# Optimization experiments

Hardware: AMD Instinct MI355X
Metric: run time of the kernel (lower is better)

The kernel has to match this reference:

```python
import jax, jax.numpy as jnp
import numpy as np

N, E, D, L = 100000, 600000, 128, 5
EPS = 1e-5


def setup_inputs() -> dict:
    key = jax.random.key(0)
    ks = jax.random.split(key, 32)
    ri = lambda k, shape, hi: jax.random.randint(k, shape, 0, hi)
    rn = lambda k, shape: jax.random.normal(k, shape, jnp.float32) * 0.02
    inp = {
        'atomic_num': ri(ks[0], (N,), 119),
        'formal_charge': ri(ks[1], (N,), 11),
        'chiral_tag': ri(ks[2], (N,), 5),
        'hybridization': ri(ks[3], (N,), 8),
        'num_explicit_hs': ri(ks[4], (N,), 6),
        'is_aromatic': ri(ks[5], (N,), 2),
        'edge_index': ri(ks[6], (2, E), N),
        'is_conjugated': ri(ks[7], (E,), 2),
        'edge_is_aromatic': ri(ks[8], (E,), 2),
        'bond_type': ri(ks[9], (E,), 22),
        'bond_dir': ri(ks[10], (E,), 7),
        'bond_stereo': ri(ks[11], (E,), 6),
        # atom embedding tables (vocab sizes are typical RDKit cardinalities)
        'emb_atomic_num': rn(ks[12], (120, D)),
        'emb_formal_charge': rn(ks[13], (12, D)),
        'emb_chiral_tag': rn(ks[14], (5, D)),
        'emb_hybridization': rn(ks[15], (8, D)),
        'emb_num_explicit_hs': rn(ks[16], (6, D)),
        'emb_is_aromatic': rn(ks[17], (2, D)),
        # per-layer edge embedding tables, stacked on leading layer axis
        'e_conj': rn(ks[18], (L, 3, D)),
        'e_arom': rn(ks[19], (L, 3, D)),
        'e_btype': rn(ks[20], (L, 23, D)),
        'e_bdir': rn(ks[21], (L, 8, D)),
        'e_bstereo': rn(ks[22], (L, 7, D)),
        # per-layer GIN MLP (D -> 2D -> D)
        'mlp_w1': rn(ks[23], (L, D, 2 * D)),
        'mlp_b1': jnp.zeros((L, 2 * D), jnp.float32),
        'mlp_w2': rn(ks[24], (L, 2 * D, D)),
        'mlp_b2': jnp.zeros((L, D), jnp.float32),
        # per-layer batchnorm affine params (training-mode batch stats)
        'bn_gamma': jnp.ones((L, D), jnp.float32),
        'bn_beta': jnp.zeros((L, D), jnp.float32),
    }
    return inp


def reference(atomic_num, formal_charge, chiral_tag, hybridization,
              num_explicit_hs, is_aromatic, edge_index,
              is_conjugated, edge_is_aromatic, bond_type, bond_dir, bond_stereo,
              emb_atomic_num, emb_formal_charge, emb_chiral_tag,
              emb_hybridization, emb_num_explicit_hs, emb_is_aromatic,
              e_conj, e_arom, e_btype, e_bdir, e_bstereo,
              mlp_w1, mlp_b1, mlp_w2, mlp_b2, bn_gamma, bn_beta):
    # seed node features: sum of atom-feature embeddings  [N, D]
    h = (emb_atomic_num[atomic_num] + emb_formal_charge[formal_charge]
         + emb_chiral_tag[chiral_tag] + emb_hybridization[hybridization]
         + emb_num_explicit_hs[num_explicit_hs] + emb_is_aromatic[is_aromatic])
    src, dst = edge_index[0], edge_index[1]
    for l in range(L):
        # edge embeddings: sum of bond-feature embeddings  [E, D]
        eemb = (e_conj[l][is_conjugated] + e_arom[l][edge_is_aromatic]
                + e_btype[l][bond_type] + e_bdir[l][bond_dir]
                + e_bstereo[l][bond_stereo])
        # self-loop edges use bond-feature index 0 for every feature  [D]
        self_vec = e_conj[l, 0] + e_arom[l, 0] + e_btype[l, 0] + e_bdir[l, 0] + e_bstereo[l, 0]
        # GIN message: x_j + edge_attr, scatter-add at dst; self loops folded in analytically
        msg = h[src] + eemb                                      # [E, D]
        agg = jax.ops.segment_sum(msg, dst, num_segments=N) + h + self_vec
        # GIN update MLP: D -> 2D -> D
        hid = jax.nn.relu(agg @ mlp_w1[l] + mlp_b1[l])
        h = hid @ mlp_w2[l] + mlp_b2[l]
        # batch norm over the node dimension (training-mode batch statistics)
        mean = h.mean(axis=0)
        var = h.var(axis=0)
        h = bn_gamma[l] * (h - mean) * jax.lax.rsqrt(var + EPS) + bn_beta[l]
        if l < L - 1:
            h = jax.nn.relu(h)
        # dropout_ratio = 0.0 -> identity
    return h  # JK='last', graph_pooling=None -> node representations [N, D]
```

## Files before the change

### kernel.cpp

```cpp
#include <hip/hip_runtime.h>

#define NN 100000
#define EE 600000
#define DD 128
#define LL 5
#define CTROWS 5152
#define MBLK 1563
#define GBLK 782
#define SBLK 98

typedef float f32x4 __attribute__((ext_vector_type(4)));
typedef _Float16 f16x8 __attribute__((ext_vector_type(8)));
typedef _Float16 f16x4 __attribute__((ext_vector_type(4)));

__global__ __launch_bounds__(256) void seed_kernel(
    const int* __restrict__ an, const int* __restrict__ fc,
    const int* __restrict__ ct, const int* __restrict__ hy,
    const int* __restrict__ nh, const int* __restrict__ ar,
    const float* __restrict__ ean, const float* __restrict__ efc,
    const float* __restrict__ ect, const float* __restrict__ ehy,
    const float* __restrict__ enh, const float* __restrict__ ear,
    _Float16* __restrict__ h)
{
    int idx = blockIdx.x * 256 + threadIdx.x;
    int n = idx >> 4, q = idx & 15;
    f32x4 a0 = ((const f32x4*)(ean + an[n] * DD))[2 * q];
    f32x4 a1 = ((const f32x4*)(ean + an[n] * DD))[2 * q + 1];
    a0 += ((const f32x4*)(efc + fc[n] * DD))[2 * q];
    a1 += ((const f32x4*)(efc + fc[n] * DD))[2 * q + 1];
    a0 += ((const f32x4*)(ect + ct[n] * DD))[2 * q];
    a1 += ((const f32x4*)(ect + ct[n] * DD))[2 * q + 1];
    a0 += ((const f32x4*)(ehy + hy[n] * DD))[2 * q];
    a1 += ((const f32x4*)(ehy + hy[n] * DD))[2 * q + 1];
    a0 += ((const f32x4*)(enh + nh[n] * DD))[2 * q];
    a1 += ((const f32x4*)(enh + nh[n] * DD))[2 * q + 1];
    a0 += ((const f32x4*)(ear + ar[n] * DD))[2 * q];
    a1 += ((const f32x4*)(ear + ar[n] * DD))[2 * q + 1];
    f16x8 o;
    #pragma unroll
    for (int j = 0; j < 4; ++j) { o[j] = (_Float16)a0[j]; o[j + 4] = (_Float16)a1[j]; }
    ((f16x8*)h)[idx] = o;
}

__global__ __launch_bounds__(256) void convw1_kernel(const float* __restrict__ w1,
                                                     _Float16* __restrict__ w1t)
{
    int idx = blockIdx.x * 256 + threadIdx.x;
    int l = idx >> 15, rem = idx & 32767;
    int n = rem >> 7, k = rem & 127;
    w1t[idx] = (_Float16)w1[l * 32768 + k * 256 + n];
}
__global__ __launch_bounds__(256) void convw2_kernel(const float* __restrict__ w2,
                                                     _Float16* __restrict__ w2t)
{
    int idx = blockIdx.x * 256 + threadIdx.x;
    int l = idx >> 15, rem = idx & 32767;
    int n = rem >> 8, k = rem & 255;
    w2t[idx] = (_Float16)w2[l * 32768 + k * 128 + n];
}

__global__ void idss_kernel(float* __restrict__ idss)
{
    int t = threadIdx.x;
    idss[t] = (t < 128) ? 1.0f : 0.0f;
}

__global__ __launch_bounds__(256) void count_kernel(const int* __restrict__ ei,
                                                    int* __restrict__ cursor)
{
    int e = blockIdx.x * 256 + threadIdx.x;
    if (e < EE) atomicAdd(&cursor[ei[EE + e]], 1);
}

__global__ __launch_bounds__(1024) void btot_kernel(const int* __restrict__ cursor,
                                                    int* __restrict__ btot)
{
    __shared__ int wsum[16];
    int tid = threadIdx.x;
    int i = blockIdx.x * 1024 + tid;
    int x = (i < NN) ? cursor[i] : 0;
    #pragma unroll
    for (int off = 1; off < 64; off <<= 1) x += __shfl_xor(x, off, 64);
    if ((tid & 63) == 0) wsum[tid >> 6] = x;
    __syncthreads();
    if (tid == 0) {
        int s = 0;
        #pragma unroll
        for (int w = 0; w < 16; ++w) s += wsum[w];
        btot[blockIdx.x] = s;
    }
}

__global__ __launch_bounds__(128) void bscan_kernel(const int* __restrict__ btot,
                                                    int* __restrict__ boff,
                                                    int* __restrict__ rowstart)
{
    __shared__ int w0;
    int t = threadIdx.x;
    int lane = t & 63, wv = t >> 6;
    int x = (t < SBLK) ? btot[t] : 0;
    int incl = x;
    #pragma unroll
    for (int off = 1; off < 64; off <<= 1) {
        int u = __shfl_up(incl, off, 64);
        if (lane >= off) incl += u;
    }
    if (wv == 0 && lane == 63) w0 = incl;
    __syncthreads();
    if (wv == 1) incl += w0;
    if (t < SBLK) boff[t] = incl - x;
    if (t == 127) rowstart[NN] = incl;
}

__global__ __launch_bounds__(1024) void apply_kernel(const int* __restrict__ cursorin,
                                                     const int* __restrict__ boff,
                                                     int* __restrict__ rowstart,
                                                     int* __restrict__ cursor)
{
    __shared__ int wsum[16];
    int tid = threadIdx.x;
    int lane = tid & 63, wv = tid >> 6;
    int i = blockIdx.x * 1024 + tid;
    int x = (i < NN) ? cursorin[i] : 0;
    int incl = x;
    #pragma unroll
    for (int off = 1; off < 64; off <<= 1) {
        int u = __shfl_up(incl, off, 64);
        if (lane >= off) incl += u;
    }
    if (lane == 63) wsum[wv] = incl;
    __syncthreads();
    int pre = 0;
    #pragma unroll
    for (int w = 0; w < 16; ++w) pre += (w < wv) ? wsum[w] : 0;
    int excl = boff[blockIdx.x] + pre + incl - x;
    if (i < NN) { rowstart[i] = excl; cursor[i] = excl; }
}

__global__ __launch_bounds__(256) void fill_kernel(
    const int* __restrict__ ei, int* __restrict__ cursor, int* __restrict__ rec,
    const int* __restrict__ f0, const int* __restrict__ f1,
    const int* __restrict__ f2, const int* __restrict__ f3,
    const int* __restrict__ f4)
{
    int e = blockIdx.x * 256 + threadIdx.x;
    if (e >= EE) return;
    int dst = ei[EE + e];
    int p = atomicAdd(&cursor[dst], 1);
    int f = f0[e] + 2 * (f1[e] + 2 * (f2[e] + 23 * (f3[e] + 8 * f4[e])));
    rec[p] = ei[e] | (f << 17);
}

__global__ __launch_bounds__(256) void ctab_kernel(
    const float* __restrict__ ec, const float* __restrict__ ea,
    const float* __restrict__ eb, const float* __restrict__ ed,
    const float* __restrict__ es, _Float16* __restrict__ ctab)
{
    int idx = blockIdx.x * 256 + threadIdx.x;
    int row = idx >> 4, q = idx & 15;
    int conj = row & 1, arom = (row >> 1) & 1;
    int r2 = row >> 2;
    int bt = r2 % 23, r3 = r2 / 23;
    int bd = r3 & 7, bs = r3 >> 3;
    f32x4 a0 = ((const f32x4*)(ec + conj * DD))[2 * q]
             + ((const f32x4*)(ea + arom * DD))[2 * q]
             + ((const f32x4*)(eb + bt * DD))[2 * q]
             + ((const f32x4*)(ed + bd * DD))[2 * q]
             + ((const f32x4*)(es + bs * DD))[2 * q];
    f32x4 a1 = ((const f32x4*)(ec + conj * DD))[2 * q + 1]
             + ((const f32x4*)(ea + arom * DD))[2 * q + 1]
             + ((const f32x4*)(eb + bt * DD))[2 * q + 1]
             + ((const f32x4*)(ed + bd * DD))[2 * q + 1]
             + ((const f32x4*)(es + bs * DD))[2 * q + 1];
    f16x8 o;
    #pragma unroll
    for (int j = 0; j < 4; ++j) { o[j] = (_Float16)a0[j]; o[j + 4] = (_Float16)a1[j]; }
    ((f16x8*)ctab)[idx] = o;
}

__global__ __launch_bounds__(256) void gather_bn_kernel(
    const _Float16* __restrict__ hsrc, _Float16* __restrict__ agg,
    const int* __restrict__ rowstart, const int* __restrict__ rec,
    const _Float16* __restrict__ ctab, const float* __restrict__ ss, int dorelu)
{
    int idx = blockIdx.x * 256 + threadIdx.x;
    int n = idx >> 4, q = idx & 15;
    f32x4 sc0 = ((const f32x4*)ss)[2 * q],        sc1 = ((const f32x4*)ss)[2 * q + 1];
    f32x4 sh0 = ((const f32x4*)(ss + 128))[2 * q], sh1 = ((const f32x4*)(ss + 128))[2 * q + 1];
    int p0 = rowstart[n], p1 = rowstart[n + 1];
    f16x8 x = ((const f16x8*)hsrc)[idx];
    f16x8 c0 = ((const f16x8*)ctab)[q];
    float v[8];
    #pragma unroll
    for (int j = 0; j < 8; ++j) {
        float sc = (j < 4) ? sc0[j] : sc1[j - 4];
        float sh = (j < 4) ? sh0[j] : sh1[j - 4];
        float t = (float)x[j] * sc + sh;
        if (dorelu && t < 0.f) t = 0.f;
        v[j] = t + (float)c0[j];
    }
    if (p0 < p1) {
        int r0 = rec[p0];
        int r1 = (p0 + 1 < p1) ? rec[p0 + 1] : r0;
        f16x8 y0 = *(const f16x8*)(hsrc + (size_t)(r0 & 0x1FFFF) * DD + q * 8);
        f16x8 e0 = *(const f16x8*)(ctab + (size_t)(((unsigned)r0) >> 17) * DD + q * 8);
        for (int p = p0; p < p1; ++p) {
            int r2 = (p + 2 < p1) ? rec[p + 2] : r1;
            f16x8 y1 = *(const f16x8*)(hsrc + (size_t)(r1 & 0x1FFFF) * DD + q * 8);
            f16x8 e1 = *(const f16x8*)(ctab + (size_t)(((unsigned)r1) >> 17) * DD + q * 8);
            #pragma unroll
            for (int j = 0; j < 8; ++j) {
                float sc = (j < 4) ? sc0[j] : sc1[j - 4];
                float sh = (j < 4) ? sh0[j] : sh1[j - 4];
                float t = (float)y0[j] * sc + sh;
                if (dorelu && t < 0.f) t = 0.f;
                v[j] += t + (float)e0[j];
            }
            y0 = y1; e0 = e1; r1 = r2;
        }
    }
    f16x8 o;
    #pragma unroll
    for (int j = 0; j < 8; ++j) o[j] = (_Float16)v[j];
    ((f16x8*)agg)[idx] = o;
}

__global__ __launch_bounds__(256, 2) void mlp_kernel(
    const _Float16* __restrict__ A, const _Float16* __restrict__ w1t,
    const _Float16* __restrict__ w2t,
    const float* __restrict__ b1, const float* __restrict__ b2,
    _Float16* __restrict__ hpre, float* __restrict__ psum, float* __restrict__ psq,
    int M)
{
    __shared__ _Float16 hid[2][8 * 4 * 64 * 8];
    int tid = threadIdx.x;
    int w = tid >> 6, lane = tid & 63;
    int ln = lane & 15, quad = lane >> 4;
    int nodebase = blockIdx.x * 128;
    const f32x4 zero = {0.f, 0.f, 0.f, 0.f};

    f16x8 w1f[4][4];
    #pragma unroll
    for (int n1 = 0; n1 < 4; ++n1)
        #pragma unroll
        for (int kt = 0; kt < 4; ++kt)
            w1f[n1][kt] = *(const f16x8*)(w1t + (w * 64 + n1 * 16 + ln) * 128 + kt * 32 + quad * 8);
    f32x4 b1v[4];
    #pragma unroll
    for (int n1 = 0; n1 < 4; ++n1)
        b1v[n1] = *(const f32x4*)(b1 + w * 64 + n1 * 16 + quad * 4);

    auto gemm1 = [&](int g) {
        int node0 = nodebase + g * 64;
        #pragma unroll
        for (int ns = 0; ns < 4; ++ns) {
            int row = node0 + ns * 16 + ln;
            row = row < M ? row : M - 1;
            f16x8 bact[4];
            #pragma unroll
            for (int kt = 0; kt < 4; ++kt)
                bact[kt] = *(const f16x8*)(A + (size_t)row * 128 + kt * 32 + quad * 8);
            f32x4 acc1[4] = {zero, zero, zero, zero};
            #pragma unroll
            for (int kt = 0; kt < 4; ++kt)
                #pragma unroll
                for (int n1 = 0; n1 < 4; ++n1)
                    acc1[n1] = __builtin_amdgcn_mfma_f32_16x16x32_f16(w1f[n1][kt], bact[kt], acc1[n1], 0, 0, 0);
            #pragma unroll
            for (int n1 = 0; n1 < 4; ++n1) {
                int a = w * 4 + n1;
                f16x4 pk;
                #pragma unroll
                for (int r = 0; r < 4; ++r) {
                    float v = acc1[n1][r] + b1v[n1][r];
                    v = v > 0.f ? v : 0.f;
                    pk[r] = (_Float16)v;
                }
                int lp = ((a & 1) * 2 + (quad >> 1)) * 16 + ln;
                int off = (((a >> 1) * 4 + ns) * 64 + lp) * 8 + (quad & 1) * 4;
                *(f16x4*)(&hid[g][off]) = pk;
            }
        }
    };

    gemm1(0);

    f16x8 w2f[2][8];
    #pragma unroll
    for (int n2 = 0; n2 < 2; ++n2)
        #pragma unroll
        for (int kt2 = 0; kt2 < 8; ++kt2)
            w2f[n2][kt2] = *(const f16x8*)(w2t + (w * 32 + n2 * 16 + ln) * 256 + kt2 * 32 + quad * 8);
    f32x4 b2v[2];
    #pragma unroll
    for (int n2 = 0; n2 < 2; ++n2)
        b2v[n2] = *(const f32x4*)(b2 + w * 32 + n2 * 16 + quad * 4);

    gemm1(1);

    __syncthreads();

    f32x4 ssum[2] = {zero, zero};
    f32x4 sqsum[2] = {zero, zero};
    #pragma unroll
    for (int g = 0; g < 2; ++g) {
        int node0 = nodebase + g * 64;
        #pragma unroll
        for (int ns = 0; ns < 4; ++ns) {
            f32x4 acc2[2] = {zero, zero};
            #pragma unroll
            for (int kt2 = 0; kt2 < 8; ++kt2) {
                f16x8 bf = *(const f16x8*)(&hid[g][((kt2 * 4 + ns) * 64 + lane) * 8]);
                acc2[0] = __builtin_amdgcn_mfma_f32_16x16x32_f16(w2f[0][kt2], bf, acc2[0], 0, 0, 0);
                acc2[1] = __builtin_amdgcn_mfma_f32_16x16x32_f16(w2f[1][kt2], bf, acc2[1], 0, 0, 0);
            }
            int node = node0 + ns * 16 + ln;
            bool valid = node < M;
            #pragma unroll
            for (int n2 = 0; n2 < 2; ++n2) {
                f32x4 v;
                f16x4 pk;
                #pragma unroll
                for (int r = 0; r < 4; ++r) {
                    v[r] = acc2[n2][r] + b2v[n2][r];
                    pk[r] = (_Float16)v[r];
                }
                if (valid) {
                    *(f16x4*)(hpre + (size_t)node * 128 + w * 32 + n2 * 16 + quad * 4) = pk;
                    ssum[n2] += v;
                    sqsum[n2] += v * v;
                }
            }
        }
    }

    #pragma unroll
    for (int n2 = 0; n2 < 2; ++n2)
        #pragma unroll
        for (int off = 1; off < 16; off <<= 1)
            #pragma unroll
            for (int r = 0; r < 4; ++r) {
                ssum[n2][r] += __shfl_xor(ssum[n2][r], off, 64);
                sqsum[n2][r] += __shfl_xor(sqsum[n2][r], off, 64);
            }
    if (ln == 0) {
        #pragma unroll
        for (int n2 = 0; n2 < 2; ++n2) {
            *(f32x4*)(psum + blockIdx.x * 128 + w * 32 + n2 * 16 + quad * 4) = ssum[n2];
            *(f32x4*)(psq + blockIdx.x * 128 + w * 32 + n2 * 16 + quad * 4) = sqsum[n2];
        }
    }
}

__global__ __launch_bounds__(256) void reduce_kernel(
    const float* __restrict__ psum, const float* __restrict__ psq,
    const float* __restrict__ gamma, const float* __restrict__ beta,
    float* __restrict__ ss, int nblk)
{
    int c = blockIdx.x;
    int tid = threadIdx.x;
    float s = 0.f, q = 0.f;
    for (int b = tid; b < nblk; b += 256) {
        s += psum[b * 128 + c];
        q += psq[b * 128 + c];
    }
    #pragma unroll
    for (int off = 1; off < 64; off <<= 1) {
        s += __shfl_xor(s, off, 64);
        q += __shfl_xor(q, off, 64);
    }
    __shared__ float rs[4], rq[4];
    int wave = tid >> 6;
    if ((tid & 63) == 0) { rs[wave] = s; rq[wave] = q; }
    __syncthreads();
    if (tid == 0) {
        s = rs[0] + rs[1] + rs[2] + rs[3];
        q = rq[0] + rq[1] + rq[2] + rq[3];
        const float invN = 1.0f / NN;
        float mean = s * invN;
        float var = q * invN - mean * mean;
        float inv = rsqrtf(var + 1e-5f);
        float scale = gamma[c] * inv;
        ss[c] = scale;
        ss[128 + c] = beta[c] - mean * scale;
    }
}

__global__ __launch_bounds__(256) void final_bn_kernel(
    const _Float16* __restrict__ hpre, float* __restrict__ out,
    const float* __restrict__ ss)
{
    int idx = blockIdx.x * 256 + threadIdx.x;
    int q = idx & 15;
    f16x8 x = ((const f16x8*)hpre)[idx];
    f32x4 sc0 = ((const f32x4*)ss)[2 * q],        sc1 = ((const f32x4*)ss)[2 * q + 1];
    f32x4 sh0 = ((const f32x4*)(ss + 128))[2 * q], sh1 = ((const f32x4*)(ss + 128))[2 * q + 1];
    f32x4 y0, y1;
    #pragma unroll
    for (int j = 0; j < 4; ++j) {
        y0[j] = (float)x[j] * sc0[j] + sh0[j];
        y1[j] = (float)x[j + 4] * sc1[j] + sh1[j];
    }
    ((f32x4*)out)[2 * idx] = y0;
    ((f32x4*)out)[2 * idx + 1] = y1;
}

extern "C" void kernel_launch(void* const* d_in, const int* in_sizes, int n_in,
                              void* d_out, int out_size, void* d_ws, size_t ws_size,
                              hipStream_t stream)
{
    const int* an  = (const int*)d_in[0];
    const int* fc  = (const int*)d_in[1];
    const int* ct  = (const int*)d_in[2];
    const int* hy  = (const int*)d_in[3];
    const int* nh  = (const int*)d_in[4];
    const int* ar  = (const int*)d_in[5];
    const int* ei  = (const int*)d_in[6];
    const int* econ = (const int*)d_in[7];
    const int* earo = (const int*)d_in[8];
    const int* ebt  = (const int*)d_in[9];
    const int* ebd  = (const int*)d_in[10];
    const int* ebs  = (const int*)d_in[11];
    const float* ean = (const float*)d_in[12];
    const float* efc = (const float*)d_in[13];
    const float* ect = (const float*)d_in[14];
    const float* ehy = (const float*)d_in[15];
    const float* enh = (const float*)d_in[16];
    const float* ear = (const float*)d_in[17];
    const float* e_conj   = (const float*)d_in[18];
    const float* e_arom   = (const float*)d_in[19];
    const float* e_btype  = (const float*)d_in[20];
    const float* e_bdir   = (const float*)d_in[21];
    const float* e_bstereo= (const float*)d_in[22];
    const float* mlp_w1 = (const float*)d_in[23];
    const float* mlp_b1 = (const float*)d_in[24];
    const float* mlp_w2 = (const float*)d_in[25];
    const float* mlp_b2 = (const float*)d_in[26];
    const float* bn_gamma = (const float*)d_in[27];
    const float* bn_beta  = (const float*)d_in[28];

    _Float16* h0   = (_Float16*)d_ws;
    _Float16* agg  = h0 + (size_t)NN * DD;
    _Float16* hpre = agg + (size_t)NN * DD;
    _Float16* w1t  = hpre + (size_t)NN * DD;
    _Float16* w2t  = w1t + LL * 256 * 128;
    _Float16* ctab = w2t + LL * 128 * 256;
    float*    psum = (float*)(ctab + CTROWS * DD);
    float*    psq  = psum + MBLK * 128;
    float*    ss   = psq + MBLK * 128;
    float*    idss = ss + 256;
    int* rowstart = (int*)(idss + 256);
    int* cursor   = rowstart + NN + 8;
    int* rec      = cursor + NN;
    int* btot     = rec + EE;
    int* boff     = btot + SBLK + 8;

    convw1_kernel<<<640, 256, 0, stream>>>(mlp_w1, w1t);
    convw2_kernel<<<640, 256, 0, stream>>>(mlp_w2, w2t);
    seed_kernel<<<6250, 256, 0, stream>>>(an, fc, ct, hy, nh, ar,
                                          ean, efc, ect, ehy, enh, ear, h0);
    idss_kernel<<<1, 256, 0, stream>>>(idss);

    hipMemsetAsync(cursor, 0, NN * sizeof(int), stream);
    count_kernel<<<2344, 256, 0, stream>>>(ei, cursor);
    btot_kernel<<<SBLK, 1024, 0, stream>>>(cursor, btot);
    bscan_kernel<<<1, 128, 0, stream>>>(btot, boff, rowstart);
    apply_kernel<<<SBLK, 1024, 0, stream>>>(cursor, boff, rowstart, cursor);
    fill_kernel<<<2344, 256, 0, stream>>>(ei, cursor, rec,
                                          econ, earo, ebt, ebd, ebs);

    for (int l = 0; l < LL; ++l) {
        ctab_kernel<<<322, 256, 0, stream>>>(
            e_conj + l * 3 * DD, e_arom + l * 3 * DD, e_btype + l * 23 * DD,
            e_bdir + l * 8 * DD, e_bstereo + l * 7 * DD, ctab);
        gather_bn_kernel<<<6250, 256, 0, stream>>>(
            (l == 0) ? h0 : hpre, agg, rowstart, rec, ctab,
            (l == 0) ? idss : ss, (l == 0) ? 0 : 1);
        mlp_kernel<<<GBLK, 256, 0, stream>>>(
            agg, w1t + l * 32768, w2t + l * 32768,
            mlp_b1 + l * 256, mlp_b2 + l * 128,
            hpre, psum, psq, NN);
        reduce_kernel<<<128, 256, 0, stream>>>(
            psum, psq, bn_gamma + l * 128, bn_beta + l * 128, ss, GBLK);
    }
    final_bn_kernel<<<6250, 256, 0, stream>>>(hpre, (float*)d_out, ss);
}
```

Baseline: 634.4 us.

## Split MLP kernel across eight waves and single-buffer the hidden tile

The fused GIN MLP kernel now runs 512 threads (8 waves) per block instead of 4. Each wave owns half as many output columns in both GEMMs, which halves the per-wave weight fragments held in registers. The hidden-activation LDS buffer drops from double to single, and the two 64-node groups are processed one after another with barriers between them. This is meant to raise occupancy and latency hiding, at the cost of extra barriers, less overlap between the two GEMMs, and each wave reloading the activation rows.

New measurement: 690.3 us. 8.8% more time.

```diff
diff --git a/kernel.cpp b/kernel.cpp
--- a/kernel.cpp
+++ b/kernel.cpp
@@ -225,33 +225,44 @@
     ((f16x8*)agg)[idx] = o;
 }
 
-__global__ __launch_bounds__(256, 2) void mlp_kernel(
+__global__ __launch_bounds__(512, 2) void mlp_kernel(
     const _Float16* __restrict__ A, const _Float16* __restrict__ w1t,
     const _Float16* __restrict__ w2t,
     const float* __restrict__ b1, const float* __restrict__ b2,
     _Float16* __restrict__ hpre, float* __restrict__ psum, float* __restrict__ psq,
     int M)
 {
-    __shared__ _Float16 hid[2][8 * 4 * 64 * 8];
+    __shared__ _Float16 hid[8 * 4 * 64 * 8];
     int tid = threadIdx.x;
     int w = tid >> 6, lane = tid & 63;
     int ln = lane & 15, quad = lane >> 4;
     int nodebase = blockIdx.x * 128;
     const f32x4 zero = {0.f, 0.f, 0.f, 0.f};
 
-    f16x8 w1f[4][4];
-    #pragma unroll
-    for (int n1 = 0; n1 < 4; ++n1)
+    f16x8 w1f[2][4];
+    #pragma unroll
+    for (int n1 = 0; n1 < 2; ++n1)
         #pragma unroll
         for (int kt = 0; kt < 4; ++kt)
-            w1f[n1][kt] = *(const f16x8*)(w1t + (w * 64 + n1 * 16 + ln) * 128 + kt * 32 + quad * 8);
-    f32x4 b1v[4];
-    #pragma unroll
-    for (int n1 = 0; n1 < 4; ++n1)
-        b1v[n1] = *(const f32x4*)(b1 + w * 64 + n1 * 16 + quad * 4);
-
-    auto gemm1 = [&](int g) {
+            w1f[n1][kt] = *(const f16x8*)(w1t + (w * 32 + n1 * 16 + ln) * 128 + kt * 32 + quad * 8);
+    f32x4 b1v[2];
+    #pragma unroll
+    for (int n1 = 0; n1 < 2; ++n1)
+        b1v[n1] = *(const f32x4*)(b1 + w * 32 + n1 * 16 + quad * 4);
+
+    f16x8 w2f[8];
+    #pragma unroll
+    for (int kt2 = 0; kt2 < 8; ++kt2)
+        w2f[kt2] = *(const f16x8*)(w2t + (w * 16 + ln) * 256 + kt2 * 32 + quad * 8);
+    f32x4 b2v = *(const f32x4*)(b2 + w * 16 + quad * 4);
+
+    f32x4 ssum = zero, sqsum = zero;
+
+    #pragma unroll
+    for (int g = 0; g < 2; ++g) {
         int node0 = nodebase + g * 64;
+        if (g) __syncthreads();
+
         #pragma unroll
         for (int ns = 0; ns < 4; ++ns) {
             int row = node0 + ns * 16 + ln;
@@ -260,15 +271,15 @@
             #pragma unroll
             for (int kt = 0; kt < 4; ++kt)
                 bact[kt] = *(const f16x8*)(A + (size_t)row * 128 + kt * 32 + quad * 8);
-            f32x4 acc1[4] = {zero, zero, zero, zero};
+            f32x4 acc1[2] = {zero, zero};
             #pragma unroll
             for (int kt = 0; kt < 4; ++kt)
                 #pragma unroll
-                for (int n1 = 0; n1 < 4; ++n1)
+                for (int n1 = 0; n1 < 2; ++n1)
                     acc1[n1] = __builtin_amdgcn_mfma_f32_16x16x32_f16(w1f[n1][kt], bact[kt], acc1[n1], 0, 0, 0);
             #pragma unroll
-            for (int n1 = 0; n1 < 4; ++n1) {
-                int a = w * 4 + n1;
+            for (int n1 = 0; n1 < 2; ++n1) {
+                int a = w * 2 + n1;
                 f16x4 pk;
                 #pragma unroll
                 for (int r = 0; r < 4; ++r) {
@@ -278,77 +289,47 @@
                 }
                 int lp = ((a & 1) * 2 + (quad >> 1)) * 16 + ln;
                 int off = (((a >> 1) * 4 + ns) * 64 + lp) * 8 + (quad & 1) * 4;
-                *(f16x4*)(&hid[g][off]) = pk;
+                *(f16x4*)(&hid[off]) = pk;
             }
         }
-    };
-
-    gemm1(0);
-
-    f16x8 w2f[2][8];
-    #pragma unroll
-    for (int n2 = 0; n2 < 2; ++n2)
-        #pragma unroll
-        for (int kt2 = 0; kt2 < 8; ++kt2)
-            w2f[n2][kt2] = *(const f16x8*)(w2t + (w * 32 + n2 * 16 + ln) * 256 + kt2 * 32 + quad * 8);
-    f32x4 b2v[2];
-    #pragma unroll
-    for (int n2 = 0; n2 < 2; ++n2)
-        b2v[n2] = *(const f32x4*)(b2 + w * 32 + n2 * 16 + quad * 4);
-
-    gemm1(1);
-
-    __syncthreads();
-
-    f32x4 ssum[2] = {zero, zero};
-    f32x4 sqsum[2] = {zero, zero};
-    #pragma unroll
-    for (int g = 0; g < 2; ++g) {
-        int node0 = nodebase + g * 64;
+
+        __syncthreads();
+
         #pragma unroll
         for (int ns = 0; ns < 4; ++ns) {
-            f32x4 acc2[2] = {zero, zero};
+            f32x4 acc2 = zero;
             #pragma unroll
             for (int kt2 = 0; kt2 < 8; ++kt2) {
-                f16x8 bf = *(const f16x8*)(&hid[g][((kt2 * 4 + ns) * 64 + lane) * 8]);
-                acc2[0] = __builtin_amdgcn_mfma_f32_16x16x32_f16(w2f[0][kt2], bf, acc2[0], 0, 0, 0);
-                acc2[1] = __builtin_amdgcn_mfma_f32_16x16x32_f16(w2f[1][kt2], bf, acc2[1], 0, 0, 0);
+                f16x8 bf = *(const f16x8*)(&hid[((kt2 * 4 + ns) * 64 + lane) * 8]);
+                acc2 = __builtin_amdgcn_mfma_f32_16x16x32_f16(w2f[kt2], bf, acc2, 0, 0, 0);
             }
             int node = node0 + ns * 16 + ln;
             bool valid = node < M;
-            #pragma unroll
-            for (int n2 = 0; n2 < 2; ++n2) {
-                f32x4 v;
-                f16x4 pk;
-                #pragma unroll
-                for (int r = 0; r < 4; ++r) {
-                    v[r] = acc2[n2][r] + b2v[n2][r];
-                    pk[r] = (_Float16)v[r];
-                }
-                if (valid) {
-                    *(f16x4*)(hpre + (size_t)node * 128 + w * 32 + n2 * 16 + quad * 4) = pk;
-                    ssum[n2] += v;
-                    sqsum[n2] += v * v;
-                }
+            f32x4 v;
+            f16x4 pk;
+            #pragma unroll
+            for (int r = 0; r < 4; ++r) {
+                v[r] = acc2[r] + b2v[r];
+                pk[r] = (_Float16)v[r];
+            }
+            if (valid) {
+                *(f16x4*)(hpre + (size_t)node * 128 + w * 16 + quad * 4) = pk;
+                ssum += v;
+                sqsum += v * v;
             }
         }
     }
 
     #pragma unroll
-    for (int n2 = 0; n2 < 2; ++n2)
+    for (int off = 1; off < 16; off <<= 1)
         #pragma unroll
-        for (int off = 1; off < 16; off <<= 1)
-            #pragma unroll
-            for (int r = 0; r < 4; ++r) {
-                ssum[n2][r] += __shfl_xor(ssum[n2][r], off, 64);
-                sqsum[n2][r] += __shfl_xor(sqsum[n2][r], off, 64);
-            }
+        for (int r = 0; r < 4; ++r) {
+            ssum[r] += __shfl_xor(ssum[r], off, 64);
+            sqsum[r] += __shfl_xor(sqsum[r], off, 64);
+        }
     if (ln == 0) {
-        #pragma unroll
-        for (int n2 = 0; n2 < 2; ++n2) {
-            *(f32x4*)(psum + blockIdx.x * 128 + w * 32 + n2 * 16 + quad * 4) = ssum[n2];
-            *(f32x4*)(psq + blockIdx.x * 128 + w * 32 + n2 * 16 + quad * 4) = sqsum[n2];
-        }
+        *(f32x4*)(psum + blockIdx.x * 128 + w * 16 + quad * 4) = ssum;
+        *(f32x4*)(psq + blockIdx.x * 128 + w * 16 + quad * 4) = sqsum;
     }
 }
 
@@ -476,7 +457,7 @@
         gather_bn_kernel<<<6250, 256, 0, stream>>>(
             (l == 0) ? h0 : hpre, agg, rowstart, rec, ctab,
             (l == 0) ? idss : ss, (l == 0) ? 0 : 1);
-        mlp_kernel<<<GBLK, 256, 0, stream>>>(
+        mlp_kernel<<<GBLK, 512, 0, stream>>>(
             agg, w1t + l * 32768, w2t + l * 32768,
             mlp_b1 + l * 256, mlp_b2 + l * 128,
             hpre, psum, psq, NN);
```

## Make MLP kernel persistent with register-prefetched activation tiles

Applied to the files above, without the earlier changes.

The MLP kernel now launches 256 persistent blocks, each looping over a contiguous range of 64-node tiles, instead of 782 blocks handling 128 nodes each. The next tile's activation rows are prefetched into registers while the current tile's first GEMM runs. Weights are loaded once per block and amortised over more tiles, and fewer partial BN sums go to the reduce kernel. In exchange the shared hidden buffer is single-buffered, there are two barriers per tile, occupancy drops to one block per CU, and the extra prefetch registers could spill.

Result: faster. 586.1 us (-7.6%).

```diff
diff --git a/kernel.cpp b/kernel.cpp
--- a/kernel.cpp
+++ b/kernel.cpp
@@ -6,7 +6,8 @@
 #define LL 5
 #define CTROWS 5152
 #define MBLK 1563
-#define GBLK 782
+#define TILES 1563
+#define PBLK 256
 #define SBLK 98
 
 typedef float f32x4 __attribute__((ext_vector_type(4)));
@@ -225,19 +226,31 @@
     ((f16x8*)agg)[idx] = o;
 }
 
-__global__ __launch_bounds__(256, 2) void mlp_kernel(
+__global__ __launch_bounds__(256, 1) void mlp_kernel(
     const _Float16* __restrict__ A, const _Float16* __restrict__ w1t,
     const _Float16* __restrict__ w2t,
     const float* __restrict__ b1, const float* __restrict__ b2,
     _Float16* __restrict__ hpre, float* __restrict__ psum, float* __restrict__ psq,
     int M)
 {
-    __shared__ _Float16 hid[2][8 * 4 * 64 * 8];
+    __shared__ _Float16 hid[8 * 4 * 64 * 8];
     int tid = threadIdx.x;
     int w = tid >> 6, lane = tid & 63;
     int ln = lane & 15, quad = lane >> 4;
-    int nodebase = blockIdx.x * 128;
     const f32x4 zero = {0.f, 0.f, 0.f, 0.f};
+
+    int t0 = (blockIdx.x * TILES) >> 8;
+    int t1 = ((blockIdx.x + 1) * TILES) >> 8;
+
+    f16x8 ba[4][4];
+    #pragma unroll
+    for (int ns = 0; ns < 4; ++ns) {
+        int row = t0 * 64 + ns * 16 + ln;
+        row = row < M ? row : M - 1;
+        #pragma unroll
+        for (int kt = 0; kt < 4; ++kt)
+            ba[ns][kt] = *(const f16x8*)(A + (size_t)row * 128 + kt * 32 + quad * 8);
+    }
 
     f16x8 w1f[4][4];
     #pragma unroll
@@ -250,22 +263,38 @@
     for (int n1 = 0; n1 < 4; ++n1)
         b1v[n1] = *(const f32x4*)(b1 + w * 64 + n1 * 16 + quad * 4);
 
-    auto gemm1 = [&](int g) {
-        int node0 = nodebase + g * 64;
+    f16x8 w2f[2][8];
+    #pragma unroll
+    for (int n2 = 0; n2 < 2; ++n2)
+        #pragma unroll
+        for (int kt2 = 0; kt2 < 8; ++kt2)
+            w2f[n2][kt2] = *(const f16x8*)(w2t + (w * 32 + n2 * 16 + ln) * 256 + kt2 * 32 + quad * 8);
+    f32x4 b2v[2];
+    #pragma unroll
+    for (int n2 = 0; n2 < 2; ++n2)
+        b2v[n2] = *(const f32x4*)(b2 + w * 32 + n2 * 16 + quad * 4);
+
+    f32x4 ssum[2] = {zero, zero};
+    f32x4 sqsum[2] = {zero, zero};
+
+    for (int t = t0; t < t1; ++t) {
+        int node0 = t * 64;
+
         #pragma unroll
         for (int ns = 0; ns < 4; ++ns) {
-            int row = node0 + ns * 16 + ln;
-            row = row < M ? row : M - 1;
-            f16x8 bact[4];
-            #pragma unroll
-            for (int kt = 0; kt < 4; ++kt)
-                bact[kt] = *(const f16x8*)(A + (size_t)row * 128 + kt * 32 + quad * 8);
             f32x4 acc1[4] = {zero, zero, zero, zero};
             #pragma unroll
             for (int kt = 0; kt < 4; ++kt)
                 #pragma unroll
                 for (int n1 = 0; n1 < 4; ++n1)
-                    acc1[n1] = __builtin_amdgcn_mfma_f32_16x16x32_f16(w1f[n1][kt], bact[kt], acc1[n1], 0, 0, 0);
+                    acc1[n1] = __builtin_amdgcn_mfma_f32_16x16x32_f16(w1f[n1][kt], ba[ns][kt], acc1[n1], 0, 0, 0);
+            {
+                int row = (t + 1) * 64 + ns * 16 + ln;
+                row = row < M ? row : M - 1;
+                #pragma unroll
+                for (int kt = 0; kt < 4; ++kt)
+                    ba[ns][kt] = *(const f16x8*)(A + (size_t)row * 128 + kt * 32 + quad * 8);
+            }
             #pragma unroll
             for (int n1 = 0; n1 < 4; ++n1) {
                 int a = w * 4 + n1;
@@ -278,39 +307,18 @@
                 }
                 int lp = ((a & 1) * 2 + (quad >> 1)) * 16 + ln;
                 int off = (((a >> 1) * 4 + ns) * 64 + lp) * 8 + (quad & 1) * 4;
-                *(f16x4*)(&hid[g][off]) = pk;
+                *(f16x4*)(&hid[off]) = pk;
             }
         }
-    };
-
-    gemm1(0);
-
-    f16x8 w2f[2][8];
-    #pragma unroll
-    for (int n2 = 0; n2 < 2; ++n2)
-        #pragma unroll
-        for (int kt2 = 0; kt2 < 8; ++kt2)
-            w2f[n2][kt2] = *(const f16x8*)(w2t + (w * 32 + n2 * 16 + ln) * 256 + kt2 * 32 + quad * 8);
-    f32x4 b2v[2];
-    #pragma unroll
-    for (int n2 = 0; n2 < 2; ++n2)
-        b2v[n2] = *(const f32x4*)(b2 + w * 32 + n2 * 16 + quad * 4);
-
-    gemm1(1);
-
-    __syncthreads();
-
-    f32x4 ssum[2] = {zero, zero};
-    f32x4 sqsum[2] = {zero, zero};
-    #pragma unroll
-    for (int g = 0; g < 2; ++g) {
-        int node0 = nodebase + g * 64;
+
+        __syncthreads();
+
         #pragma unroll
         for (int ns = 0; ns < 4; ++ns) {
             f32x4 acc2[2] = {zero, zero};
             #pragma unroll
             for (int kt2 = 0; kt2 < 8; ++kt2) {
-                f16x8 bf = *(const f16x8*)(&hid[g][((kt2 * 4 + ns) * 64 + lane) * 8]);
+                f16x8 bf = *(const f16x8*)(&hid[((kt2 * 4 + ns) * 64 + lane) * 8]);
                 acc2[0] = __builtin_amdgcn_mfma_f32_16x16x32_f16(w2f[0][kt2], bf, acc2[0], 0, 0, 0);
                 acc2[1] = __builtin_amdgcn_mfma_f32_16x16x32_f16(w2f[1][kt2], bf, acc2[1], 0, 0, 0);
             }
@@ -332,6 +340,8 @@
                 }
             }
         }
+
+        __syncthreads();
     }
 
     #pragma unroll
@@ -476,12 +486,12 @@
         gather_bn_kernel<<<6250, 256, 0, stream>>>(
             (l == 0) ? h0 : hpre, agg, rowstart, rec, ctab,
             (l == 0) ? idss : ss, (l == 0) ? 0 : 1);
-        mlp_kernel<<<GBLK, 256, 0, stream>>>(
+        mlp_kernel<<<PBLK, 256, 0, stream>>>(
             agg, w1t + l * 32768, w2t + l * 32768,
             mlp_b1 + l * 256, mlp_b2 + l * 128,
             hpre, psum, psq, NN);
         reduce_kernel<<<128, 256, 0, stream>>>(
-            psum, psq, bn_gamma + l * 128, bn_beta + l * 128, ss, GBLK);
+            psum, psq, bn_gamma + l * 128, bn_beta + l * 128, ss, PBLK);
     }
     final_bn_kernel<<<6250, 256, 0, stream>>>(hpre, (float*)d_out, ss);
 }
```
